# Optimization experiments

Hardware: AMD Instinct MI355X
Metric: run time of the kernel (lower is better)

Reference implementation:

```python
import jax, jax.numpy as jnp
import numpy as np
import math

B, C, N = 8, 128, 16384
H = 4
DK = C // H
COUT = 128
EPS = 1e-5

def _ln(x, g, b):
    # x: (B,H,N,DK); g,b: (H,DK) -> per-head LayerNorm over last dim
    mu = jnp.mean(x, axis=-1, keepdims=True)
    var = jnp.mean((x - mu) ** 2, axis=-1, keepdims=True)
    xh = (x - mu) / jnp.sqrt(var + EPS)
    return xh * g[None, :, None, :] + b[None, :, None, :]

def setup_inputs() -> dict:
    key = jax.random.key(0)
    ks = jax.random.split(key, 12)
    s = 0.02
    return {
        "x": jax.random.normal(ks[0], (B, C, N), jnp.float32),
        "Wq": jax.random.normal(ks[1], (C, C), jnp.float32) * s + 0.01 * jnp.eye(C),
        "bq": jnp.zeros((C,), jnp.float32),
        "Wk": jax.random.normal(ks[2], (C, C), jnp.float32) * s + 0.01 * jnp.eye(C),
        "bk": jnp.zeros((C,), jnp.float32),
        "Wv": jax.random.normal(ks[3], (C, C), jnp.float32) * s + 0.01 * jnp.eye(C),
        "bv": jnp.zeros((C,), jnp.float32),
        "gK": jnp.ones((H, DK), jnp.float32),
        "bK": jnp.zeros((H, DK), jnp.float32),
        "gV": jnp.ones((H, DK), jnp.float32),
        "bV": jnp.zeros((H, DK), jnp.float32),
        "Wo": jax.random.normal(ks[4], (COUT, C), jnp.float32) * s,
        "bo": jnp.zeros((COUT,), jnp.float32),
    }

def reference(x, Wq, bq, Wk, bk, Wv, bv, gK, bK, gV, bV, Wo, bo):
    # x: (B, C, N) -> (B, N, C)
    xt = jnp.transpose(x, (0, 2, 1))
    def proj(W, b):
        y = xt @ W.T + b                      # (B,N,C)
        return jnp.transpose(y.reshape(B, N, H, DK), (0, 2, 1, 3))  # (B,H,N,DK)
    q = proj(Wq, bq)
    k = proj(Wk, bk)
    v = proj(Wv, bv)
    # galerkin: per-head LayerNorm on K and V (vectorized over heads)
    k = _ln(k, gK, bK)
    v = _ln(v, gV, bV)
    # linear (no-softmax) attention: (Q K^T / sqrt(dk)) / N @ V == Q @ (K^T V) / (sqrt(dk)*N)
    # dropout from F.dropout is treated as identity (deterministic reference)
    kv = jnp.einsum("bhnd,bhne->bhde", k, v)            # (B,H,DK,DK)
    attn = jnp.einsum("bhnd,bhde->bhne", q, kv) / (math.sqrt(DK) * N)
    out = jnp.transpose(attn, (0, 2, 1, 3)).reshape(B, N, C)  # merge heads
    out = out @ Wo.T + bo                                # (B,N,COUT)
    return jnp.transpose(out, (0, 2, 1))                 # (B,COUT,N)
```

## Files before the change

### kernel.cpp

```cpp
#include <hip/hip_runtime.h>
#include <cmath>

#define BB 8
#define CC 128
#define NN 16384
#define HH 4
#define NBK 64
#define SX 272

typedef __attribute__((ext_vector_type(8))) short bf16x8;
typedef __attribute__((ext_vector_type(4))) float f32x4;

#define MFMA(a, b, c) __builtin_amdgcn_mfma_f32_16x16x32_bf16(a, b, c, 0, 0, 0)

__device__ __forceinline__ unsigned short f2b(float f) {
  union { float f; unsigned u; } v; v.f = f;
  unsigned r = v.u + 0x7FFFu + ((v.u >> 16) & 1u);
  return (unsigned short)(r >> 16);
}

__device__ __forceinline__ int xt_addr(int n, int cblk) {
  return n * SX + ((cblk ^ ((n >> 2) & 7)) << 4);
}
__device__ __forceinline__ int kt_byte(int c, int n) {
  return c * 144 + ((((n >> 3) ^ (c & 7)) << 4) | ((n & 7) << 1));
}

__global__ void k_prep(const float* __restrict__ Wq, const float* __restrict__ Wk,
                       const float* __restrict__ Wv, const float* __restrict__ Wo,
                       unsigned short* __restrict__ Wb) {
  const int idx = blockIdx.x * 256 + threadIdx.x;
  const int which = idx >> 14;
  const float* src = (which == 0) ? Wq : (which == 1) ? Wk : (which == 2) ? Wv : Wo;
  Wb[idx] = f2b(src[idx & 16383]);
}

__global__ __launch_bounds__(512, 4)
void k_fuse1(const float* __restrict__ x,
             const unsigned short* __restrict__ Wkb, const unsigned short* __restrict__ Wvb,
             const float* __restrict__ bk, const float* __restrict__ bv,
             const float* __restrict__ gK, const float* __restrict__ bK,
             const float* __restrict__ gV, const float* __restrict__ bV,
             float* __restrict__ kvp) {
  extern __shared__ char lds[];
  char* KT = lds + 34816;
  char* VT = lds + 53248;
  float* KVS = (float*)lds;

  const int tid = threadIdx.x;
  const int lane = tid & 63;
  const int w = tid >> 6;
  const int b = blockIdx.y;
  const int bx = blockIdx.x;
  const int l15 = lane & 15, l4 = lane >> 4;

  const int ph = w >> 1, pp = w & 1;
  const int kh = w >> 1, khalf = w & 1;

  const unsigned short* Wsrc = pp ? Wvb : Wkb;
  bf16x8 wf[2][4];
#pragma unroll
  for (int mf = 0; mf < 2; ++mf)
#pragma unroll
    for (int ks = 0; ks < 4; ++ks)
      wf[mf][ks] = *(const bf16x8*)(Wsrc + (ph * 32 + mf * 16 + l15) * 128 + ks * 32 + l4 * 8);

  float bias[2][4], gam[2][4], bet[2][4];
  {
    const float* bsrc = pp ? bv : bk;
    const float* gsrc = pp ? gV : gK;
    const float* esrc = pp ? bV : bK;
#pragma unroll
    for (int mf = 0; mf < 2; ++mf)
#pragma unroll
      for (int r = 0; r < 4; ++r) {
        const int cg = ph * 32 + mf * 16 + l4 * 4 + r;
        bias[mf][r] = bsrc[cg]; gam[mf][r] = gsrc[cg]; bet[mf][r] = esrc[cg];
      }
  }

  f32x4 kvacc[2][2];
#pragma unroll
  for (int i = 0; i < 2; ++i)
#pragma unroll
    for (int j = 0; j < 2; ++j) kvacc[i][j] = (f32x4){0.f, 0.f, 0.f, 0.f};

  const int half2 = lane >> 5;
  const int cb2 = w * 2 + half2;
  const int nn = (lane & 31) * 2;
  const float* xrow = x + ((size_t)b * CC + cb2 * 8) * NN + bx * 256 + nn;

  float2 rx[8];
#pragma unroll
  for (int cc = 0; cc < 8; ++cc) rx[cc] = *(const float2*)(xrow + (size_t)cc * NN);

  for (int it = 0; it < 4; ++it) {
    char* XT = (it & 1) ? (lds + 17408) : lds;

#pragma unroll
    for (int j = 0; j < 2; ++j) {
      const int n = nn + j;
      bf16x8 pk;
#pragma unroll
      for (int cc = 0; cc < 8; ++cc)
        ((unsigned short*)&pk)[cc] = f2b(j ? rx[cc].y : rx[cc].x);
      *(bf16x8*)(XT + n * SX + ((cb2 ^ ((n >> 2) & 7)) << 4)) = pk;
    }
    if (it < 3) {
      const float* xn = xrow + (it + 1) * 64;
#pragma unroll
      for (int cc = 0; cc < 8; ++cc) rx[cc] = *(const float2*)(xn + (size_t)cc * NN);
    }
    __syncthreads();

    char* DST = pp ? VT : KT;
#pragma unroll
    for (int nf = 0; nf < 4; ++nf) {
      const int n = nf * 16 + l15;
      f32x4 a0 = (f32x4){0.f, 0.f, 0.f, 0.f}, a1 = (f32x4){0.f, 0.f, 0.f, 0.f};
#pragma unroll
      for (int ks = 0; ks < 4; ++ks) {
        const bf16x8 xf = *(const bf16x8*)(XT + xt_addr(n, ks * 4 + l4));
        a0 = MFMA(wf[0][ks], xf, a0);
        a1 = MFMA(wf[1][ks], xf, a1);
      }
#pragma unroll
      for (int r = 0; r < 4; ++r) { a0[r] += bias[0][r]; a1[r] += bias[1][r]; }
      float s = 0.f, ss = 0.f;
#pragma unroll
      for (int r = 0; r < 4; ++r) {
        s += a0[r] + a1[r];
        ss += a0[r] * a0[r] + a1[r] * a1[r];
      }
      s += __shfl_xor(s, 16); ss += __shfl_xor(ss, 16);
      s += __shfl_xor(s, 32); ss += __shfl_xor(ss, 32);
      const float mu = s * (1.f / 32.f);
      const float var = ss * (1.f / 32.f) - mu * mu;
      const float rstd = rsqrtf(var + 1e-5f);
#pragma unroll
      for (int r = 0; r < 4; ++r) {
        const int c0k = ph * 32 + l4 * 4 + r;
        *(unsigned short*)(DST + kt_byte(c0k, n)) =
            f2b((a0[r] - mu) * rstd * gam[0][r] + bet[0][r]);
        const int c1k = ph * 32 + 16 + l4 * 4 + r;
        *(unsigned short*)(DST + kt_byte(c1k, n)) =
            f2b((a1[r] - mu) * rstd * gam[1][r] + bet[1][r]);
      }
    }
    __syncthreads();

#pragma unroll
    for (int mf = 0; mf < 2; ++mf) {
      const int ck = kh * 32 + mf * 16 + l15;
      const bf16x8 ka = *(const bf16x8*)(KT + ck * 144 + (((khalf * 4 + l4) ^ (ck & 7)) << 4));
#pragma unroll
      for (int ef = 0; ef < 2; ++ef) {
        const int cv = kh * 32 + ef * 16 + l15;
        const bf16x8 vb = *(const bf16x8*)(VT + cv * 144 + (((khalf * 4 + l4) ^ (cv & 7)) << 4));
        kvacc[mf][ef] = MFMA(ka, vb, kvacc[mf][ef]);
      }
    }
  }

  __syncthreads();
#pragma unroll
  for (int mf = 0; mf < 2; ++mf)
#pragma unroll
    for (int ef = 0; ef < 2; ++ef)
#pragma unroll
      for (int r = 0; r < 4; ++r) {
        const int d = mf * 16 + l4 * 4 + r, e = ef * 16 + l15;
        KVS[w * 1024 + d * 32 + e] = kvacc[mf][ef][r];
      }
  __syncthreads();
  {
    float* og = kvp + ((size_t)(b * NBK + bx)) * 8192;
#pragma unroll
    for (int i = 0; i < 4; ++i) {
      const int off = i * 2048 + tid * 4;
      *(f32x4*)(og + off) = *(const f32x4*)(KVS + off);
    }
  }
}

__global__ void k_reduceA(const float* __restrict__ kvp, float* __restrict__ p2) {
  const int blk = blockIdx.x;
  const int s = blk & 7, h = (blk >> 3) & 3, b = blk >> 5;
  const int t = threadIdx.x;
  f32x4 acc = (f32x4){0.f, 0.f, 0.f, 0.f};
  for (int i = 0; i < 8; ++i) {
    const int bx = s * 8 + i;
    const float* base = kvp + ((size_t)(b * NBK + bx)) * 8192 + t * 4;
    acc += *(const f32x4*)(base + (2 * h) * 1024);
    acc += *(const f32x4*)(base + (2 * h + 1) * 1024);
  }
  *(f32x4*)(p2 + (size_t)blk * 1024 + t * 4) = acc;
}

__global__ void k_reduceB(const float* __restrict__ p2, unsigned short* __restrict__ kvT,
                          const float scale) {
  const int bh = blockIdx.x;
  const int t = threadIdx.x;
  f32x4 acc = (f32x4){0.f, 0.f, 0.f, 0.f};
  for (int s = 0; s < 8; ++s)
    acc += *(const f32x4*)(p2 + ((size_t)bh * 8 + s) * 1024 + t * 4);
#pragma unroll
  for (int j = 0; j < 4; ++j) {
    const int i = t * 4 + j;
    const int d = i >> 5, e = i & 31;
    kvT[(size_t)bh * 1024 + e * 32 + d] = f2b(acc[j] * scale);
  }
}

__global__ __launch_bounds__(512, 4)
void k_pass2(const float* __restrict__ x,
             const unsigned short* __restrict__ Wqb, const float* __restrict__ bq,
             const unsigned short* __restrict__ kvT,
             const unsigned short* __restrict__ Wob, const float* __restrict__ bo,
             float* __restrict__ out) {
  extern __shared__ char lds[];
  char* QS = lds + 34816;
  char* AS = lds + 51200;

  const int tid = threadIdx.x;
  const int lane = tid & 63;
  const int w = tid >> 6;
  const int b = blockIdx.y;
  const int l15 = lane & 15, l4 = lane >> 4;
  const int h = w >> 1, half = w & 1;

  bf16x8 kvf[2];
#pragma unroll
  for (int mf = 0; mf < 2; ++mf)
    kvf[mf] = *(const bf16x8*)(kvT + (((size_t)b * HH + h) * 32 + mf * 16 + l15) * 32 + l4 * 8);
  bf16x8 wq[4], wo[4];
#pragma unroll
  for (int ks = 0; ks < 4; ++ks) {
    wq[ks] = *(const bf16x8*)(Wqb + (w * 16 + l15) * 128 + ks * 32 + l4 * 8);
    wo[ks] = *(const bf16x8*)(Wob + (w * 16 + l15) * 128 + ks * 32 + l4 * 8);
  }
  float bq_r[4], bo_r[4];
#pragma unroll
  for (int r = 0; r < 4; ++r) {
    bq_r[r] = bq[w * 16 + l4 * 4 + r];
    bo_r[r] = bo[w * 16 + l4 * 4 + r];
  }

  const int half2 = lane >> 5;
  const int cb2 = w * 2 + half2;
  const int nn = (lane & 31) * 2;
  const float* xrow = x + ((size_t)b * CC + cb2 * 8) * NN + blockIdx.x * 256 + nn;
  float* ob = out + (size_t)b * CC * NN;

  float2 rx[8];
#pragma unroll
  for (int cc = 0; cc < 8; ++cc) rx[cc] = *(const float2*)(xrow + (size_t)cc * NN);

  for (int it = 0; it < 4; ++it) {
    const int n0 = blockIdx.x * 256 + it * 64;
    char* XT = (it & 1) ? (lds + 17408) : lds;

#pragma unroll
    for (int j = 0; j < 2; ++j) {
      const int n = nn + j;
      bf16x8 pk;
#pragma unroll
      for (int cc = 0; cc < 8; ++cc)
        ((unsigned short*)&pk)[cc] = f2b(j ? rx[cc].y : rx[cc].x);
      *(bf16x8*)(XT + n * SX + ((cb2 ^ ((n >> 2) & 7)) << 4)) = pk;
    }
    if (it < 3) {
      const float* xn = xrow + (it + 1) * 64;
#pragma unroll
      for (int cc = 0; cc < 8; ++cc) rx[cc] = *(const float2*)(xn + (size_t)cc * NN);
    }
    __syncthreads();

    f32x4 qa[4];
#pragma unroll
    for (int nf = 0; nf < 4; ++nf) qa[nf] = (f32x4){0.f, 0.f, 0.f, 0.f};
#pragma unroll
    for (int ks = 0; ks < 4; ++ks)
#pragma unroll
      for (int nf = 0; nf < 4; ++nf) {
        const int n = nf * 16 + l15;
        const bf16x8 xf = *(const bf16x8*)(XT + xt_addr(n, ks * 4 + l4));
        qa[nf] = MFMA(wq[ks], xf, qa[nf]);
      }
#pragma unroll
    for (int nf = 0; nf < 4; ++nf) {
      const int n = nf * 16 + l15;
      const int c0 = w * 16 + l4 * 4;
      unsigned long long pk = 0;
#pragma unroll
      for (int r = 0; r < 4; ++r)
        pk |= (unsigned long long)f2b(qa[nf][r] + bq_r[r]) << (16 * r);
      *(unsigned long long*)(QS + n * 256 + (((c0 >> 3) ^ (n & 15)) << 4) + ((c0 & 7) << 1)) = pk;
    }
    __syncthreads();

    f32x4 aa[2][2];
#pragma unroll
    for (int i = 0; i < 2; ++i)
#pragma unroll
      for (int j = 0; j < 2; ++j) aa[i][j] = (f32x4){0.f, 0.f, 0.f, 0.f};
    bf16x8 qf[2];
#pragma unroll
    for (int nf = 0; nf < 2; ++nf) {
      const int n = half * 32 + nf * 16 + l15;
      const int cq = h * 32 + l4 * 8;
      qf[nf] = *(const bf16x8*)(QS + n * 256 + ((((cq >> 3)) ^ (n & 15)) << 4));
    }
#pragma unroll
    for (int mf = 0; mf < 2; ++mf)
#pragma unroll
      for (int nf = 0; nf < 2; ++nf) aa[mf][nf] = MFMA(kvf[mf], qf[nf], aa[mf][nf]);
#pragma unroll
    for (int mf = 0; mf < 2; ++mf)
#pragma unroll
      for (int nf = 0; nf < 2; ++nf) {
        const int n = half * 32 + nf * 16 + l15;
        const int e0 = h * 32 + mf * 16 + l4 * 4;
        unsigned long long pk = 0;
#pragma unroll
        for (int r = 0; r < 4; ++r)
          pk |= (unsigned long long)f2b(aa[mf][nf][r]) << (16 * r);
        *(unsigned long long*)(AS + n * 256 + (((e0 >> 3) ^ (n & 15)) << 4) + ((e0 & 7) << 1)) = pk;
      }
    __syncthreads();

    f32x4 oa[4];
#pragma unroll
    for (int nf = 0; nf < 4; ++nf) oa[nf] = (f32x4){0.f, 0.f, 0.f, 0.f};
#pragma unroll
    for (int ks = 0; ks < 4; ++ks)
#pragma unroll
      for (int nf = 0; nf < 4; ++nf) {
        const int n = nf * 16 + l15;
        const bf16x8 af = *(const bf16x8*)(AS + n * 256 + (((ks * 4 + l4) ^ (n & 15)) << 4));
        oa[nf] = MFMA(wo[ks], af, oa[nf]);
      }
#pragma unroll
    for (int nf = 0; nf < 4; ++nf)
#pragma unroll
      for (int r = 0; r < 4; ++r) {
        const int c = w * 16 + l4 * 4 + r;
        ob[(size_t)c * NN + n0 + nf * 16 + l15] = oa[nf][r] + bo_r[r];
      }
  }
}

extern "C" void kernel_launch(void* const* d_in, const int* in_sizes, int n_in,
                              void* d_out, int out_size, void* d_ws, size_t ws_size,
                              hipStream_t stream) {
  const float* x  = (const float*)d_in[0];
  const float* Wq = (const float*)d_in[1];
  const float* bq = (const float*)d_in[2];
  const float* Wk = (const float*)d_in[3];
  const float* bk = (const float*)d_in[4];
  const float* Wv = (const float*)d_in[5];
  const float* bv = (const float*)d_in[6];
  const float* gK = (const float*)d_in[7];
  const float* bK = (const float*)d_in[8];
  const float* gV = (const float*)d_in[9];
  const float* bV = (const float*)d_in[10];
  const float* Wo = (const float*)d_in[11];
  const float* bo = (const float*)d_in[12];
  float* out = (float*)d_out;

  char* ws = (char*)d_ws;
  float* kvp = (float*)ws;
  float* p2  = kvp + (size_t)BB * NBK * 8192;
  unsigned short* kvTb = (unsigned short*)(p2 + 256 * 1024);
  unsigned short* Wb = kvTb + (size_t)BB * HH * 1024;
  const unsigned short* Wqb = Wb;
  const unsigned short* Wkb = Wb + 16384;
  const unsigned short* Wvb = Wb + 32768;
  const unsigned short* Wob = Wb + 49152;

  (void)hipFuncSetAttribute(reinterpret_cast<const void*>(k_fuse1),
                            hipFuncAttributeMaxDynamicSharedMemorySize, 71680);
  (void)hipFuncSetAttribute(reinterpret_cast<const void*>(k_pass2),
                            hipFuncAttributeMaxDynamicSharedMemorySize, 67584);

  k_prep<<<256, 256, 0, stream>>>(Wq, Wk, Wv, Wo, Wb);

  k_fuse1<<<dim3(NBK, BB), 512, 71680, stream>>>(
      x, Wkb, Wvb, bk, bv, gK, bK, gV, bV, kvp);

  k_reduceA<<<256, 256, 0, stream>>>(kvp, p2);

  const float scale = 1.0f / (5.65685424949238f * 16384.0f);
  k_reduceB<<<32, 256, 0, stream>>>(p2, kvTb, scale);

  k_pass2<<<dim3(NBK, BB), 512, 67584, stream>>>(
      x, Wqb, bq, kvTb, Wob, bo, out);
}
```

Baseline: 81.52 us.

## Load x in 128-column tiles without register prefetch double-buffering

Restructures k_fuse1's x staging. It no longer prefetches the next 64-column chunk into registers while computing on a double-buffered LDS tile. Instead it loads 128 columns at once into a single LDS buffer (one wave lane per 2 columns), then runs two 64-column projection/LayerNorm/KV sub-steps with a barrier after each. This cuts register pressure and the number of x-load/convert rounds, but it gives up the overlap of global loads with compute and adds barriers.

```diff
diff --git a/kernel.cpp b/kernel.cpp
--- a/kernel.cpp
+++ b/kernel.cpp
@@ -43,6 +43,7 @@
              const float* __restrict__ gV, const float* __restrict__ bV,
              float* __restrict__ kvp) {
   extern __shared__ char lds[];
+  char* XT = lds;
   char* KT = lds + 34816;
   char* VT = lds + 53248;
   float* KVS = (float*)lds;
@@ -85,84 +86,82 @@
 #pragma unroll
     for (int j = 0; j < 2; ++j) kvacc[i][j] = (f32x4){0.f, 0.f, 0.f, 0.f};
 
-  const int half2 = lane >> 5;
-  const int cb2 = w * 2 + half2;
-  const int nn = (lane & 31) * 2;
-  const float* xrow = x + ((size_t)b * CC + cb2 * 8) * NN + bx * 256 + nn;
-
-  float2 rx[8];
-#pragma unroll
-  for (int cc = 0; cc < 8; ++cc) rx[cc] = *(const float2*)(xrow + (size_t)cc * NN);
-
-  for (int it = 0; it < 4; ++it) {
-    char* XT = (it & 1) ? (lds + 17408) : lds;
-
-#pragma unroll
-    for (int j = 0; j < 2; ++j) {
-      const int n = nn + j;
-      bf16x8 pk;
-#pragma unroll
-      for (int cc = 0; cc < 8; ++cc)
-        ((unsigned short*)&pk)[cc] = f2b(j ? rx[cc].y : rx[cc].x);
-      *(bf16x8*)(XT + n * SX + ((cb2 ^ ((n >> 2) & 7)) << 4)) = pk;
-    }
-    if (it < 3) {
-      const float* xn = xrow + (it + 1) * 64;
-#pragma unroll
-      for (int cc = 0; cc < 8; ++cc) rx[cc] = *(const float2*)(xn + (size_t)cc * NN);
+  for (int ot = 0; ot < 2; ++ot) {
+    const int n0 = (bx * 2 + ot) * 128;
+
+#pragma unroll
+    for (int g = 0; g < 2; ++g) {
+      const int cb = w * 2 + g;
+      const float* xb = x + ((size_t)b * CC + cb * 8) * NN + n0 + lane * 2;
+      float2 va[8];
+#pragma unroll
+      for (int cc = 0; cc < 8; ++cc) va[cc] = *(const float2*)(xb + (size_t)cc * NN);
+#pragma unroll
+      for (int j = 0; j < 2; ++j) {
+        const int n = lane * 2 + j;
+        bf16x8 pk;
+#pragma unroll
+        for (int cc = 0; cc < 8; ++cc)
+          ((unsigned short*)&pk)[cc] = f2b(j ? va[cc].y : va[cc].x);
+        *(bf16x8*)(XT + n * SX + ((cb ^ ((n >> 2) & 7)) << 4)) = pk;
+      }
     }
     __syncthreads();
 
-    char* DST = pp ? VT : KT;
-#pragma unroll
-    for (int nf = 0; nf < 4; ++nf) {
-      const int n = nf * 16 + l15;
-      f32x4 a0 = (f32x4){0.f, 0.f, 0.f, 0.f}, a1 = (f32x4){0.f, 0.f, 0.f, 0.f};
-#pragma unroll
-      for (int ks = 0; ks < 4; ++ks) {
-        const bf16x8 xf = *(const bf16x8*)(XT + xt_addr(n, ks * 4 + l4));
-        a0 = MFMA(wf[0][ks], xf, a0);
-        a1 = MFMA(wf[1][ks], xf, a1);
-      }
-#pragma unroll
-      for (int r = 0; r < 4; ++r) { a0[r] += bias[0][r]; a1[r] += bias[1][r]; }
-      float s = 0.f, ss = 0.f;
-#pragma unroll
-      for (int r = 0; r < 4; ++r) {
-        s += a0[r] + a1[r];
-        ss += a0[r] * a0[r] + a1[r] * a1[r];
-      }
-      s += __shfl_xor(s, 16); ss += __shfl_xor(ss, 16);
-      s += __shfl_xor(s, 32); ss += __shfl_xor(ss, 32);
-      const float mu = s * (1.f / 32.f);
-      const float var = ss * (1.f / 32.f) - mu * mu;
-      const float rstd = rsqrtf(var + 1e-5f);
-#pragma unroll
-      for (int r = 0; r < 4; ++r) {
-        const int c0k = ph * 32 + l4 * 4 + r;
-        *(unsigned short*)(DST + kt_byte(c0k, n)) =
-            f2b((a0[r] - mu) * rstd * gam[0][r] + bet[0][r]);
-        const int c1k = ph * 32 + 16 + l4 * 4 + r;
-        *(unsigned short*)(DST + kt_byte(c1k, n)) =
-            f2b((a1[r] - mu) * rstd * gam[1][r] + bet[1][r]);
-      }
-    }
-    __syncthreads();
-
-#pragma unroll
-    for (int mf = 0; mf < 2; ++mf) {
-      const int ck = kh * 32 + mf * 16 + l15;
-      const bf16x8 ka = *(const bf16x8*)(KT + ck * 144 + (((khalf * 4 + l4) ^ (ck & 7)) << 4));
-#pragma unroll
-      for (int ef = 0; ef < 2; ++ef) {
-        const int cv = kh * 32 + ef * 16 + l15;
-        const bf16x8 vb = *(const bf16x8*)(VT + cv * 144 + (((khalf * 4 + l4) ^ (cv & 7)) << 4));
-        kvacc[mf][ef] = MFMA(ka, vb, kvacc[mf][ef]);
-      }
-    }
-  }
-
-  __syncthreads();
+    for (int t = 0; t < 2; ++t) {
+      const int nbase = t * 64;
+      char* DST = pp ? VT : KT;
+#pragma unroll
+      for (int nf = 0; nf < 4; ++nf) {
+        const int n = nbase + nf * 16 + l15;
+        f32x4 a0 = (f32x4){0.f, 0.f, 0.f, 0.f}, a1 = (f32x4){0.f, 0.f, 0.f, 0.f};
+#pragma unroll
+        for (int ks = 0; ks < 4; ++ks) {
+          const bf16x8 xf = *(const bf16x8*)(XT + xt_addr(n, ks * 4 + l4));
+          a0 = MFMA(wf[0][ks], xf, a0);
+          a1 = MFMA(wf[1][ks], xf, a1);
+        }
+#pragma unroll
+        for (int r = 0; r < 4; ++r) { a0[r] += bias[0][r]; a1[r] += bias[1][r]; }
+        float s = 0.f, ss = 0.f;
+#pragma unroll
+        for (int r = 0; r < 4; ++r) {
+          s += a0[r] + a1[r];
+          ss += a0[r] * a0[r] + a1[r] * a1[r];
+        }
+        s += __shfl_xor(s, 16); ss += __shfl_xor(ss, 16);
+        s += __shfl_xor(s, 32); ss += __shfl_xor(ss, 32);
+        const float mu = s * (1.f / 32.f);
+        const float var = ss * (1.f / 32.f) - mu * mu;
+        const float rstd = rsqrtf(var + 1e-5f);
+        const int nloc = nf * 16 + l15;
+#pragma unroll
+        for (int r = 0; r < 4; ++r) {
+          const int c0k = ph * 32 + l4 * 4 + r;
+          *(unsigned short*)(DST + kt_byte(c0k, nloc)) =
+              f2b((a0[r] - mu) * rstd * gam[0][r] + bet[0][r]);
+          const int c1k = ph * 32 + 16 + l4 * 4 + r;
+          *(unsigned short*)(DST + kt_byte(c1k, nloc)) =
+              f2b((a1[r] - mu) * rstd * gam[1][r] + bet[1][r]);
+        }
+      }
+      __syncthreads();
+
+#pragma unroll
+      for (int mf = 0; mf < 2; ++mf) {
+        const int ck = kh * 32 + mf * 16 + l15;
+        const bf16x8 ka = *(const bf16x8*)(KT + ck * 144 + (((khalf * 4 + l4) ^ (ck & 7)) << 4));
+#pragma unroll
+        for (int ef = 0; ef < 2; ++ef) {
+          const int cv = kh * 32 + ef * 16 + l15;
+          const bf16x8 vb = *(const bf16x8*)(VT + cv * 144 + (((khalf * 4 + l4) ^ (cv & 7)) << 4));
+          kvacc[mf][ef] = MFMA(ka, vb, kvacc[mf][ef]);
+        }
+      }
+      __syncthreads();
+    }
+  }
+
 #pragma unroll
   for (int mf = 0; mf < 2; ++mf)
 #pragma unroll
```

Measured after the change: 73.50 us. -9.8%, faster.
